# Kernel optimization log

Measured on AMD Instinct MI355X. Metric: run time of the kernel, lower is better.

## Reference

```python
import jax, jax.numpy as jnp
import numpy as np

NUM_GRAPHS = 256
LAMBDA = 0.01


def setup_inputs() -> dict:
    key = jax.random.key(0)
    k1, k2, k3, k4, k5 = jax.random.split(key, 5)
    N, D, E = 100000, 64, 1200000
    logits = jax.random.normal(k1, (NUM_GRAPHS, 10), dtype=jnp.float32)
    labels = jax.random.randint(k2, (NUM_GRAPHS,), 0, 10, dtype=jnp.int64)
    x = jax.random.normal(k3, (N, D), dtype=jnp.float32)
    edge_index = jax.random.randint(k4, (2, E), 0, N, dtype=jnp.int64)
    batch = jnp.sort(jax.random.randint(k5, (N,), 0, NUM_GRAPHS, dtype=jnp.int64))
    return {"logits": logits, "labels": labels, "x": x,
            "edge_index": edge_index, "batch": batch}


def reference(logits, labels, x, edge_index, batch):
    # cross-entropy (mean over graphs)
    logp = jax.nn.log_softmax(logits, axis=-1)
    ce_loss = -jnp.mean(jnp.take_along_axis(logp, labels[:, None], axis=1))

    # Dirichlet energy
    row, col = edge_index[0], edge_index[1]
    N = x.shape[0]
    ones_e = jnp.ones(row.shape, dtype=x.dtype)
    deg = jax.ops.segment_sum(ones_e, row, num_segments=N)          # [N]
    deg_inv_sqrt = jnp.where(deg > 0, jax.lax.rsqrt(jnp.where(deg > 0, deg, 1.0)), 0.0)
    norm = deg_inv_sqrt[row] * deg_inv_sqrt[col]                    # [E]
    diff = x[row] - x[col]                                          # [E, D]
    sq = jnp.sum(diff * diff, axis=1)                               # [E]
    energy_e = norm * sq

    seg = batch[row]                                                # graph id per edge
    energy_sum = jax.ops.segment_sum(energy_e, seg, num_segments=NUM_GRAPHS)
    edge_counts = jax.ops.segment_sum(ones_e, seg, num_segments=NUM_GRAPHS)
    edge_counts = jnp.clip(edge_counts, 1.0, None)
    smoothness_loss = jnp.mean(energy_sum / edge_counts)

    return ce_loss + LAMBDA * smoothness_loss
```

## Files before the change

kernel.cpp:

```cpp
#include <hip/hip_runtime.h>
#include <math.h>

#define NUM_GRAPHS 256
#define LAMBDA 0.01f

typedef int            v4i __attribute__((ext_vector_type(4)));
typedef float          v4f __attribute__((ext_vector_type(4)));
typedef unsigned int   v4u __attribute__((ext_vector_type(4)));
typedef unsigned short v8h __attribute__((ext_vector_type(8)));

__device__ __forceinline__ unsigned short f2bf_rne(float f) {
    unsigned int u = __float_as_uint(f);
    u = u + 0x7fffu + ((u >> 16) & 1u);
    return (unsigned short)(u >> 16);
}

__device__ __forceinline__ float bfdiff_sq(v4u a, v4u b) {
    float s = 0.0f;
    #pragma unroll
    for (int k = 0; k < 4; ++k) {
        float alo = __uint_as_float(a[k] << 16);
        float ahi = __uint_as_float(a[k] & 0xffff0000u);
        float blo = __uint_as_float(b[k] << 16);
        float bhi = __uint_as_float(b[k] & 0xffff0000u);
        float d1 = alo - blo;
        float d2 = ahi - bhi;
        s += d1 * d1;
        s += d2 * d2;
    }
    return s;
}

__global__ void k_cvt(const float* __restrict__ x, v8h* __restrict__ xh,
                      float* __restrict__ zr, int zcount8, long total8) {
    long j = (long)blockIdx.x * blockDim.x + threadIdx.x;
    if (j < total8) {
        const v4f* xp = (const v4f*)(x + j * 8);
        v4f a = xp[0], b = xp[1];
        v8h o;
        o[0] = f2bf_rne(a[0]); o[1] = f2bf_rne(a[1]);
        o[2] = f2bf_rne(a[2]); o[3] = f2bf_rne(a[3]);
        o[4] = f2bf_rne(b[0]); o[5] = f2bf_rne(b[1]);
        o[6] = f2bf_rne(b[2]); o[7] = f2bf_rne(b[3]);
        __builtin_nontemporal_store(o, xh + j);
    }
    if (j < zcount8) {
        v4f z = {0.0f, 0.0f, 0.0f, 0.0f};
        v4f* zp = (v4f*)(zr + j * 8);
        zp[0] = z; zp[1] = z;
    }
}

__global__ void k_deg_v(const int* __restrict__ row, float* __restrict__ deg, int E) {
    const int i = blockIdx.x * blockDim.x + threadIdx.x;
    const int stride = gridDim.x * blockDim.x;
    const int E4 = E >> 2;
    const v4i* r4 = (const v4i*)row;
    for (int k = i; k < E4; k += stride) {
        v4i v = __builtin_nontemporal_load(&r4[k]);
        atomicAdd(&deg[v[0]], 1.0f);
        atomicAdd(&deg[v[1]], 1.0f);
        atomicAdd(&deg[v[2]], 1.0f);
        atomicAdd(&deg[v[3]], 1.0f);
    }
    for (int e = (E4 << 2) + i; e < E; e += stride) {
        atomicAdd(&deg[row[e]], 1.0f);
    }
}

template <bool PACK>
__global__ void k_dis(float* __restrict__ deg_dis, const int* __restrict__ batch,
                      float* __restrict__ cnt, float2* __restrict__ pk, int N) {
    int i = blockIdx.x * blockDim.x + threadIdx.x;
    bool valid = (i < N);
    float d = valid ? deg_dis[i] : 0.0f;
    int g = valid ? batch[i] : -1;
    float dis = (d > 0.0f) ? rsqrtf(d) : 0.0f;
    if (valid) {
        deg_dis[i] = dis;
        if (PACK) pk[i] = make_float2(dis, __int_as_float(g));
    }

    int gmin = g, gmax = g;
    #pragma unroll
    for (int m = 1; m < 64; m <<= 1) {
        gmin = min(gmin, __shfl_xor(gmin, m));
        gmax = max(gmax, __shfl_xor(gmax, m));
    }
    if (gmin == gmax && gmin >= 0) {
        float s = d;
        #pragma unroll
        for (int m = 1; m < 64; m <<= 1) s += __shfl_xor(s, m);
        if ((threadIdx.x & 63) == 0) atomicAdd(&cnt[g], s);
    } else if (valid) {
        atomicAdd(&cnt[g], d);
    }
}

__global__ void k_fused(const int* __restrict__ row, const int* __restrict__ col,
                        const v4u* __restrict__ xh4, const float2* __restrict__ pk,
                        float* __restrict__ g_energy, int E) {
    __shared__ float lbin[NUM_GRAPHS];
    lbin[threadIdx.x] = 0.0f;
    __syncthreads();

    const int lane   = threadIdx.x & 63;
    const int lane8  = lane & 7;
    const int gi     = lane >> 3;
    const int wave   = (blockIdx.x * blockDim.x + threadIdx.x) >> 6;
    const int nwaves = (gridDim.x * blockDim.x) >> 6;
    const int E32    = E >> 5;

    for (int t = wave; t < E32; t += nwaves) {
        const int ebase = t * 32 + gi * 4;

        v4i rv = __builtin_nontemporal_load((const v4i*)(row + ebase));
        v4i cv = __builtin_nontemporal_load((const v4i*)(col + ebase));

        v4u a0 = xh4[(long)rv[0] * 8 + lane8];
        v4u b0 = xh4[(long)cv[0] * 8 + lane8];
        v4u a1 = xh4[(long)rv[1] * 8 + lane8];
        v4u b1 = xh4[(long)cv[1] * 8 + lane8];
        v4u a2 = xh4[(long)rv[2] * 8 + lane8];
        v4u b2 = xh4[(long)cv[2] * 8 + lane8];
        v4u a3 = xh4[(long)rv[3] * 8 + lane8];
        v4u b3 = xh4[(long)cv[3] * 8 + lane8];

        float s0 = bfdiff_sq(a0, b0);
        float s1 = bfdiff_sq(a1, b1);
        float s2 = bfdiff_sq(a2, b2);
        float s3 = bfdiff_sq(a3, b3);

        s0 += __shfl_xor(s0, 1); s1 += __shfl_xor(s1, 1);
        s2 += __shfl_xor(s2, 1); s3 += __shfl_xor(s3, 1);
        s0 += __shfl_xor(s0, 2); s1 += __shfl_xor(s1, 2);
        s2 += __shfl_xor(s2, 2); s3 += __shfl_xor(s3, 2);
        s0 += __shfl_xor(s0, 4); s1 += __shfl_xor(s1, 4);
        s2 += __shfl_xor(s2, 4); s3 += __shfl_xor(s3, 4);

        if (lane8 < 4) {
            int r = rv[lane8];
            int c = cv[lane8];
            float s = (lane8 == 0) ? s0 : (lane8 == 1) ? s1 : (lane8 == 2) ? s2 : s3;
            float2 pr = pk[r];
            float2 pc = pk[c];
            atomicAdd(&lbin[__float_as_int(pr.y)], pr.x * pc.x * s);
        }
    }

    for (int e = (E32 << 5) + wave; e < E; e += nwaves) {
        int r = row[e], c = col[e];
        v4u a = xh4[(long)r * 8 + lane8];
        v4u b = xh4[(long)c * 8 + lane8];
        float s = bfdiff_sq(a, b);
        s += __shfl_xor(s, 1);
        s += __shfl_xor(s, 2);
        s += __shfl_xor(s, 4);
        if (lane == 0) {
            float2 pr = pk[r];
            float2 pc = pk[c];
            atomicAdd(&lbin[__float_as_int(pr.y)], pr.x * pc.x * s);
        }
    }

    __syncthreads();
    float v = lbin[threadIdx.x];
    if (v != 0.0f) atomicAdd(&g_energy[threadIdx.x], v);
}

__global__ void k_deg_sq(const int* __restrict__ row, const int* __restrict__ col,
                         const float4* __restrict__ x4, float* __restrict__ deg,
                         float* __restrict__ sq, int E) {
    const int lane   = threadIdx.x & 63;
    const int lane16 = lane & 15;
    const int wave   = (blockIdx.x * blockDim.x + threadIdx.x) >> 6;
    const int nwaves = (gridDim.x * blockDim.x) >> 6;
    const int gi     = (lane >> 4);
    const int E16    = E >> 4;

    for (int t = wave; t < E16; t += nwaves) {
        const int ebase = t * 16 + gi * 4;

        v4i rv = __builtin_nontemporal_load((const v4i*)(row + ebase));
        v4i cv = __builtin_nontemporal_load((const v4i*)(col + ebase));

        float4 a0 = x4[(long)rv[0] * 16 + lane16];
        float4 b0 = x4[(long)cv[0] * 16 + lane16];
        float4 a1 = x4[(long)rv[1] * 16 + lane16];
        float4 b1 = x4[(long)cv[1] * 16 + lane16];
        float4 a2 = x4[(long)rv[2] * 16 + lane16];
        float4 b2 = x4[(long)cv[2] * 16 + lane16];
        float4 a3 = x4[(long)rv[3] * 16 + lane16];
        float4 b3 = x4[(long)cv[3] * 16 + lane16];

        float dx, dy, dz, dw;
        dx = a0.x - b0.x; dy = a0.y - b0.y; dz = a0.z - b0.z; dw = a0.w - b0.w;
        float s0 = dx * dx + dy * dy + dz * dz + dw * dw;
        dx = a1.x - b1.x; dy = a1.y - b1.y; dz = a1.z - b1.z; dw = a1.w - b1.w;
        float s1 = dx * dx + dy * dy + dz * dz + dw * dw;
        dx = a2.x - b2.x; dy = a2.y - b2.y; dz = a2.z - b2.z; dw = a2.w - b2.w;
        float s2 = dx * dx + dy * dy + dz * dz + dw * dw;
        dx = a3.x - b3.x; dy = a3.y - b3.y; dz = a3.z - b3.z; dw = a3.w - b3.w;
        float s3 = dx * dx + dy * dy + dz * dz + dw * dw;

        s0 += __shfl_xor(s0, 1); s1 += __shfl_xor(s1, 1);
        s2 += __shfl_xor(s2, 1); s3 += __shfl_xor(s3, 1);
        s0 += __shfl_xor(s0, 2); s1 += __shfl_xor(s1, 2);
        s2 += __shfl_xor(s2, 2); s3 += __shfl_xor(s3, 2);
        s0 += __shfl_xor(s0, 4); s1 += __shfl_xor(s1, 4);
        s2 += __shfl_xor(s2, 4); s3 += __shfl_xor(s3, 4);
        s0 += __shfl_xor(s0, 8); s1 += __shfl_xor(s1, 8);
        s2 += __shfl_xor(s2, 8); s3 += __shfl_xor(s3, 8);

        if (lane16 == 0) {
            v4f sv;
            sv[0] = s0; sv[1] = s1; sv[2] = s2; sv[3] = s3;
            __builtin_nontemporal_store(sv, (v4f*)(sq + ebase));
        } else if (lane16 == 1) {
            atomicAdd(&deg[rv[0]], 1.0f);
        } else if (lane16 == 2) {
            atomicAdd(&deg[rv[1]], 1.0f);
        } else if (lane16 == 3) {
            atomicAdd(&deg[rv[2]], 1.0f);
        } else if (lane16 == 4) {
            atomicAdd(&deg[rv[3]], 1.0f);
        }
    }

    for (int e = (E16 << 4) + wave; e < E; e += nwaves) {
        int r = row[e], c = col[e];
        float4 a = x4[(long)r * 16 + lane16];
        float4 b = x4[(long)c * 16 + lane16];
        float dx = a.x - b.x, dy = a.y - b.y, dz = a.z - b.z, dw = a.w - b.w;
        float s = dx * dx + dy * dy + dz * dz + dw * dw;
        s += __shfl_xor(s, 1);
        s += __shfl_xor(s, 2);
        s += __shfl_xor(s, 4);
        s += __shfl_xor(s, 8);
        if (lane == 0) sq[e] = s;
        if (lane == 1) atomicAdd(&deg[r], 1.0f);
    }
}

__global__ void k_bin(const int* __restrict__ row, const int* __restrict__ col,
                      const float* __restrict__ sq, const float2* __restrict__ pk,
                      float* __restrict__ g_energy, int E) {
    __shared__ float lbin[NUM_GRAPHS];
    lbin[threadIdx.x] = 0.0f;
    __syncthreads();

    const int i = blockIdx.x * blockDim.x + threadIdx.x;
    const int stride = gridDim.x * blockDim.x;
    const int E4 = E >> 2;
    const v4i* r4 = (const v4i*)row;
    const v4i* c4 = (const v4i*)col;
    const v4f* s4 = (const v4f*)sq;

    for (int k = i; k < E4; k += stride) {
        v4i r = __builtin_nontemporal_load(&r4[k]);
        v4i c = __builtin_nontemporal_load(&c4[k]);
        v4f s = __builtin_nontemporal_load(&s4[k]);
        float2 pr0 = pk[r[0]], pr1 = pk[r[1]], pr2 = pk[r[2]], pr3 = pk[r[3]];
        float2 pc0 = pk[c[0]], pc1 = pk[c[1]], pc2 = pk[c[2]], pc3 = pk[c[3]];
        atomicAdd(&lbin[__float_as_int(pr0.y)], pr0.x * pc0.x * s[0]);
        atomicAdd(&lbin[__float_as_int(pr1.y)], pr1.x * pc1.x * s[1]);
        atomicAdd(&lbin[__float_as_int(pr2.y)], pr2.x * pc2.x * s[2]);
        atomicAdd(&lbin[__float_as_int(pr3.y)], pr3.x * pc3.x * s[3]);
    }
    for (int e = (E4 << 2) + i; e < E; e += stride) {
        float2 pr = pk[row[e]], pc = pk[col[e]];
        atomicAdd(&lbin[__float_as_int(pr.y)], pr.x * pc.x * sq[e]);
    }

    __syncthreads();
    float v = lbin[threadIdx.x];
    if (v != 0.0f) atomicAdd(&g_energy[threadIdx.x], v);
}

__global__ void k_final(const float* __restrict__ logits, const int* __restrict__ labels,
                        const float* __restrict__ g_energy, const float* __restrict__ cnt,
                        float* __restrict__ out) {
    const int t = threadIdx.x;
    const float* lg = logits + t * 10;

    float m = -INFINITY;
    #pragma unroll
    for (int j = 0; j < 10; ++j) m = fmaxf(m, lg[j]);
    float sum = 0.0f;
    #pragma unroll
    for (int j = 0; j < 10; ++j) sum += expf(lg[j] - m);
    float lse = m + logf(sum);
    float ce = lse - lg[labels[t]];

    float sm = g_energy[t] / fmaxf(cnt[t], 1.0f);

    float v = ce + LAMBDA * sm;
    #pragma unroll
    for (int mk = 1; mk < 64; mk <<= 1) v += __shfl_xor(v, mk);

    __shared__ float wsum[4];
    if ((t & 63) == 0) wsum[t >> 6] = v;
    __syncthreads();
    if (t == 0) out[0] = (wsum[0] + wsum[1] + wsum[2] + wsum[3]) * (1.0f / 256.0f);
}

extern "C" void kernel_launch(void* const* d_in, const int* in_sizes, int n_in,
                              void* d_out, int out_size, void* d_ws, size_t ws_size,
                              hipStream_t stream) {
    const float* logits = (const float*)d_in[0];
    const int* labels   = (const int*)d_in[1];
    const float* x      = (const float*)d_in[2];
    const int* edge_idx = (const int*)d_in[3];
    const int* batch    = (const int*)d_in[4];

    const int N = in_sizes[2] / 64;
    const int E = in_sizes[3] / 2;

    const int* row = edge_idx;
    const int* col = edge_idx + E;

    float*  deg_dis  = (float*)d_ws;
    float*  g_energy = deg_dis + N;
    float*  cnt      = g_energy + NUM_GRAPHS;
    float2* pk_fast  = (float2*)(cnt + NUM_GRAPHS);
    unsigned short* xh = (unsigned short*)(pk_fast + N);

    const size_t base_floats = (size_t)N + 2 * NUM_GRAPHS;
    const size_t need_fast = (base_floats + (size_t)2 * N + (size_t)32 * N) * sizeof(float);

    float*  sq      = (float*)(cnt + NUM_GRAPHS);
    float2* pk_slow = (float2*)(sq + E);
    const size_t need_sq = (base_floats + (size_t)E) * sizeof(float);
    const size_t need_pk = need_sq + (size_t)2 * N * sizeof(float);

    if (ws_size >= need_fast) {
        const long total8 = (long)N * 8;
        const int zcount8 = (int)((N + 2 * NUM_GRAPHS + 7) / 8);
        const int cvt_blocks = (int)((total8 + 255) / 256);
        k_cvt<<<cvt_blocks, 256, 0, stream>>>(x, (v8h*)xh, deg_dis, zcount8, total8);
        k_deg_v<<<1024, 256, 0, stream>>>(row, deg_dis, E);
        k_dis<true><<<(N + 255) / 256, 256, 0, stream>>>(deg_dis, batch, cnt, pk_fast, N);
        k_fused<<<2048, 256, 0, stream>>>(row, col, (const v4u*)xh, pk_fast,
                                          g_energy, E);
    } else if (ws_size >= need_pk) {
        (void)hipMemsetAsync(d_ws, 0, base_floats * sizeof(float), stream);
        k_deg_sq<<<2048, 256, 0, stream>>>(row, col, (const float4*)x, deg_dis, sq, E);
        k_dis<true><<<(N + 255) / 256, 256, 0, stream>>>(deg_dis, batch, cnt, pk_slow, N);
        k_bin<<<512, 256, 0, stream>>>(row, col, sq, pk_slow, g_energy, E);
    } else {
        (void)hipMemsetAsync(d_ws, 0, base_floats * sizeof(float), stream);
        k_deg_v<<<1024, 256, 0, stream>>>(row, deg_dis, E);
        k_dis<false><<<(N + 255) / 256, 256, 0, stream>>>(deg_dis, batch, cnt, pk_slow, N);
        k_bin<<<512, 256, 0, stream>>>(row, col, sq, pk_slow, g_energy, E);
    }
    k_final<<<1, 256, 0, stream>>>(logits, labels, g_energy, cnt, (float*)d_out);
}
```

Before: 247.1 us.

## Fuse degree counting into bf16 gather pass, bin energy in separate pass

The fast path used to run a row-only degree atomic pass and then a fused gather+energy kernel. It now computes squared differences from the bf16 copy of x together with the degree atomics in one k_gather kernel, processing 8 edges per lane group. The per-edge sums go to a workspace array that k_bin later scales and bins. This drops the separate degree pass but adds a write and re-read of an E-sized float array plus a second read of row/col. It also needs more workspace, so the fast path is only taken if ws_size covers sq as well.

```diff
diff --git a/kernel.cpp b/kernel.cpp
--- a/kernel.cpp
+++ b/kernel.cpp
@@ -51,20 +51,85 @@
     }
 }
 
-__global__ void k_deg_v(const int* __restrict__ row, float* __restrict__ deg, int E) {
-    const int i = blockIdx.x * blockDim.x + threadIdx.x;
-    const int stride = gridDim.x * blockDim.x;
-    const int E4 = E >> 2;
-    const v4i* r4 = (const v4i*)row;
-    for (int k = i; k < E4; k += stride) {
-        v4i v = __builtin_nontemporal_load(&r4[k]);
-        atomicAdd(&deg[v[0]], 1.0f);
-        atomicAdd(&deg[v[1]], 1.0f);
-        atomicAdd(&deg[v[2]], 1.0f);
-        atomicAdd(&deg[v[3]], 1.0f);
-    }
-    for (int e = (E4 << 2) + i; e < E; e += stride) {
-        atomicAdd(&deg[row[e]], 1.0f);
+__global__ void __launch_bounds__(256, 4)
+k_gather(const int* __restrict__ row, const int* __restrict__ col,
+         const v4u* __restrict__ xh4, float* __restrict__ deg,
+         float* __restrict__ sq, int E) {
+    const int lane   = threadIdx.x & 63;
+    const int lane8  = lane & 7;
+    const int gi     = lane >> 3;
+    const int wave   = (blockIdx.x * blockDim.x + threadIdx.x) >> 6;
+    const int nwaves = (gridDim.x * blockDim.x) >> 6;
+    const int E64    = E >> 6;
+
+    for (int t = wave; t < E64; t += nwaves) {
+        const int ebase = t * 64 + gi * 8;
+
+        v4i rv0 = __builtin_nontemporal_load((const v4i*)(row + ebase));
+        v4i rv1 = __builtin_nontemporal_load((const v4i*)(row + ebase + 4));
+        v4i cv0 = __builtin_nontemporal_load((const v4i*)(col + ebase));
+        v4i cv1 = __builtin_nontemporal_load((const v4i*)(col + ebase + 4));
+
+        v4u a0 = xh4[(long)rv0[0] * 8 + lane8];
+        v4u b0 = xh4[(long)cv0[0] * 8 + lane8];
+        v4u a1 = xh4[(long)rv0[1] * 8 + lane8];
+        v4u b1 = xh4[(long)cv0[1] * 8 + lane8];
+        v4u a2 = xh4[(long)rv0[2] * 8 + lane8];
+        v4u b2 = xh4[(long)cv0[2] * 8 + lane8];
+        v4u a3 = xh4[(long)rv0[3] * 8 + lane8];
+        v4u b3 = xh4[(long)cv0[3] * 8 + lane8];
+        v4u a4 = xh4[(long)rv1[0] * 8 + lane8];
+        v4u b4 = xh4[(long)cv1[0] * 8 + lane8];
+        v4u a5 = xh4[(long)rv1[1] * 8 + lane8];
+        v4u b5 = xh4[(long)cv1[1] * 8 + lane8];
+        v4u a6 = xh4[(long)rv1[2] * 8 + lane8];
+        v4u b6 = xh4[(long)cv1[2] * 8 + lane8];
+        v4u a7 = xh4[(long)rv1[3] * 8 + lane8];
+        v4u b7 = xh4[(long)cv1[3] * 8 + lane8];
+
+        float s0 = bfdiff_sq(a0, b0);
+        float s1 = bfdiff_sq(a1, b1);
+        float s2 = bfdiff_sq(a2, b2);
+        float s3 = bfdiff_sq(a3, b3);
+        float s4 = bfdiff_sq(a4, b4);
+        float s5 = bfdiff_sq(a5, b5);
+        float s6 = bfdiff_sq(a6, b6);
+        float s7 = bfdiff_sq(a7, b7);
+
+        s0 += __shfl_xor(s0, 1); s1 += __shfl_xor(s1, 1);
+        s2 += __shfl_xor(s2, 1); s3 += __shfl_xor(s3, 1);
+        s4 += __shfl_xor(s4, 1); s5 += __shfl_xor(s5, 1);
+        s6 += __shfl_xor(s6, 1); s7 += __shfl_xor(s7, 1);
+        s0 += __shfl_xor(s0, 2); s1 += __shfl_xor(s1, 2);
+        s2 += __shfl_xor(s2, 2); s3 += __shfl_xor(s3, 2);
+        s4 += __shfl_xor(s4, 2); s5 += __shfl_xor(s5, 2);
+        s6 += __shfl_xor(s6, 2); s7 += __shfl_xor(s7, 2);
+        s0 += __shfl_xor(s0, 4); s1 += __shfl_xor(s1, 4);
+        s2 += __shfl_xor(s2, 4); s3 += __shfl_xor(s3, 4);
+        s4 += __shfl_xor(s4, 4); s5 += __shfl_xor(s5, 4);
+        s6 += __shfl_xor(s6, 4); s7 += __shfl_xor(s7, 4);
+
+        if (lane8 == 0) {
+            v4f sv; sv[0] = s0; sv[1] = s1; sv[2] = s2; sv[3] = s3;
+            __builtin_nontemporal_store(sv, (v4f*)(sq + ebase));
+        } else if (lane8 == 1) {
+            v4f sv; sv[0] = s4; sv[1] = s5; sv[2] = s6; sv[3] = s7;
+            __builtin_nontemporal_store(sv, (v4f*)(sq + ebase + 4));
+        }
+        int rr = (lane8 < 4) ? rv0[lane8] : rv1[lane8 - 4];
+        atomicAdd(&deg[rr], 1.0f);
+    }
+
+    for (int e = (E64 << 6) + wave; e < E; e += nwaves) {
+        int r = row[e], c = col[e];
+        v4u a = xh4[(long)r * 8 + lane8];
+        v4u b = xh4[(long)c * 8 + lane8];
+        float s = bfdiff_sq(a, b);
+        s += __shfl_xor(s, 1);
+        s += __shfl_xor(s, 2);
+        s += __shfl_xor(s, 4);
+        if (lane == 0) sq[e] = s;
+        if (lane == 8) atomicAdd(&deg[r], 1.0f);
     }
 }
 
@@ -97,151 +162,6 @@
     }
 }
 
-__global__ void k_fused(const int* __restrict__ row, const int* __restrict__ col,
-                        const v4u* __restrict__ xh4, const float2* __restrict__ pk,
-                        float* __restrict__ g_energy, int E) {
-    __shared__ float lbin[NUM_GRAPHS];
-    lbin[threadIdx.x] = 0.0f;
-    __syncthreads();
-
-    const int lane   = threadIdx.x & 63;
-    const int lane8  = lane & 7;
-    const int gi     = lane >> 3;
-    const int wave   = (blockIdx.x * blockDim.x + threadIdx.x) >> 6;
-    const int nwaves = (gridDim.x * blockDim.x) >> 6;
-    const int E32    = E >> 5;
-
-    for (int t = wave; t < E32; t += nwaves) {
-        const int ebase = t * 32 + gi * 4;
-
-        v4i rv = __builtin_nontemporal_load((const v4i*)(row + ebase));
-        v4i cv = __builtin_nontemporal_load((const v4i*)(col + ebase));
-
-        v4u a0 = xh4[(long)rv[0] * 8 + lane8];
-        v4u b0 = xh4[(long)cv[0] * 8 + lane8];
-        v4u a1 = xh4[(long)rv[1] * 8 + lane8];
-        v4u b1 = xh4[(long)cv[1] * 8 + lane8];
-        v4u a2 = xh4[(long)rv[2] * 8 + lane8];
-        v4u b2 = xh4[(long)cv[2] * 8 + lane8];
-        v4u a3 = xh4[(long)rv[3] * 8 + lane8];
-        v4u b3 = xh4[(long)cv[3] * 8 + lane8];
-
-        float s0 = bfdiff_sq(a0, b0);
-        float s1 = bfdiff_sq(a1, b1);
-        float s2 = bfdiff_sq(a2, b2);
-        float s3 = bfdiff_sq(a3, b3);
-
-        s0 += __shfl_xor(s0, 1); s1 += __shfl_xor(s1, 1);
-        s2 += __shfl_xor(s2, 1); s3 += __shfl_xor(s3, 1);
-        s0 += __shfl_xor(s0, 2); s1 += __shfl_xor(s1, 2);
-        s2 += __shfl_xor(s2, 2); s3 += __shfl_xor(s3, 2);
-        s0 += __shfl_xor(s0, 4); s1 += __shfl_xor(s1, 4);
-        s2 += __shfl_xor(s2, 4); s3 += __shfl_xor(s3, 4);
-
-        if (lane8 < 4) {
-            int r = rv[lane8];
-            int c = cv[lane8];
-            float s = (lane8 == 0) ? s0 : (lane8 == 1) ? s1 : (lane8 == 2) ? s2 : s3;
-            float2 pr = pk[r];
-            float2 pc = pk[c];
-            atomicAdd(&lbin[__float_as_int(pr.y)], pr.x * pc.x * s);
-        }
-    }
-
-    for (int e = (E32 << 5) + wave; e < E; e += nwaves) {
-        int r = row[e], c = col[e];
-        v4u a = xh4[(long)r * 8 + lane8];
-        v4u b = xh4[(long)c * 8 + lane8];
-        float s = bfdiff_sq(a, b);
-        s += __shfl_xor(s, 1);
-        s += __shfl_xor(s, 2);
-        s += __shfl_xor(s, 4);
-        if (lane == 0) {
-            float2 pr = pk[r];
-            float2 pc = pk[c];
-            atomicAdd(&lbin[__float_as_int(pr.y)], pr.x * pc.x * s);
-        }
-    }
-
-    __syncthreads();
-    float v = lbin[threadIdx.x];
-    if (v != 0.0f) atomicAdd(&g_energy[threadIdx.x], v);
-}
-
-__global__ void k_deg_sq(const int* __restrict__ row, const int* __restrict__ col,
-                         const float4* __restrict__ x4, float* __restrict__ deg,
-                         float* __restrict__ sq, int E) {
-    const int lane   = threadIdx.x & 63;
-    const int lane16 = lane & 15;
-    const int wave   = (blockIdx.x * blockDim.x + threadIdx.x) >> 6;
-    const int nwaves = (gridDim.x * blockDim.x) >> 6;
-    const int gi     = (lane >> 4);
-    const int E16    = E >> 4;
-
-    for (int t = wave; t < E16; t += nwaves) {
-        const int ebase = t * 16 + gi * 4;
-
-        v4i rv = __builtin_nontemporal_load((const v4i*)(row + ebase));
-        v4i cv = __builtin_nontemporal_load((const v4i*)(col + ebase));
-
-        float4 a0 = x4[(long)rv[0] * 16 + lane16];
-        float4 b0 = x4[(long)cv[0] * 16 + lane16];
-        float4 a1 = x4[(long)rv[1] * 16 + lane16];
-        float4 b1 = x4[(long)cv[1] * 16 + lane16];
-        float4 a2 = x4[(long)rv[2] * 16 + lane16];
-        float4 b2 = x4[(long)cv[2] * 16 + lane16];
-        float4 a3 = x4[(long)rv[3] * 16 + lane16];
-        float4 b3 = x4[(long)cv[3] * 16 + lane16];
-
-        float dx, dy, dz, dw;
-        dx = a0.x - b0.x; dy = a0.y - b0.y; dz = a0.z - b0.z; dw = a0.w - b0.w;
-        float s0 = dx * dx + dy * dy + dz * dz + dw * dw;
-        dx = a1.x - b1.x; dy = a1.y - b1.y; dz = a1.z - b1.z; dw = a1.w - b1.w;
-        float s1 = dx * dx + dy * dy + dz * dz + dw * dw;
-        dx = a2.x - b2.x; dy = a2.y - b2.y; dz = a2.z - b2.z; dw = a2.w - b2.w;
-        float s2 = dx * dx + dy * dy + dz * dz + dw * dw;
-        dx = a3.x - b3.x; dy = a3.y - b3.y; dz = a3.z - b3.z; dw = a3.w - b3.w;
-        float s3 = dx * dx + dy * dy + dz * dz + dw * dw;
-
-        s0 += __shfl_xor(s0, 1); s1 += __shfl_xor(s1, 1);
-        s2 += __shfl_xor(s2, 1); s3 += __shfl_xor(s3, 1);
-        s0 += __shfl_xor(s0, 2); s1 += __shfl_xor(s1, 2);
-        s2 += __shfl_xor(s2, 2); s3 += __shfl_xor(s3, 2);
-        s0 += __shfl_xor(s0, 4); s1 += __shfl_xor(s1, 4);
-        s2 += __shfl_xor(s2, 4); s3 += __shfl_xor(s3, 4);
-        s0 += __shfl_xor(s0, 8); s1 += __shfl_xor(s1, 8);
-        s2 += __shfl_xor(s2, 8); s3 += __shfl_xor(s3, 8);
-
-        if (lane16 == 0) {
-            v4f sv;
-            sv[0] = s0; sv[1] = s1; sv[2] = s2; sv[3] = s3;
-            __builtin_nontemporal_store(sv, (v4f*)(sq + ebase));
-        } else if (lane16 == 1) {
-            atomicAdd(&deg[rv[0]], 1.0f);
-        } else if (lane16 == 2) {
-            atomicAdd(&deg[rv[1]], 1.0f);
-        } else if (lane16 == 3) {
-            atomicAdd(&deg[rv[2]], 1.0f);
-        } else if (lane16 == 4) {
-            atomicAdd(&deg[rv[3]], 1.0f);
-        }
-    }
-
-    for (int e = (E16 << 4) + wave; e < E; e += nwaves) {
-        int r = row[e], c = col[e];
-        float4 a = x4[(long)r * 16 + lane16];
-        float4 b = x4[(long)c * 16 + lane16];
-        float dx = a.x - b.x, dy = a.y - b.y, dz = a.z - b.z, dw = a.w - b.w;
-        float s = dx * dx + dy * dy + dz * dz + dw * dw;
-        s += __shfl_xor(s, 1);
-        s += __shfl_xor(s, 2);
-        s += __shfl_xor(s, 4);
-        s += __shfl_xor(s, 8);
-        if (lane == 0) sq[e] = s;
-        if (lane == 1) atomicAdd(&deg[r], 1.0f);
-    }
-}
-
 __global__ void k_bin(const int* __restrict__ row, const int* __restrict__ col,
                       const float* __restrict__ sq, const float2* __restrict__ pk,
                       float* __restrict__ g_energy, int E) {
@@ -277,6 +197,45 @@
     if (v != 0.0f) atomicAdd(&g_energy[threadIdx.x], v);
 }
 
+__global__ void k_deg_f(const int* __restrict__ row, float* __restrict__ deg, int E) {
+    const int i = blockIdx.x * blockDim.x + threadIdx.x;
+    const int stride = gridDim.x * blockDim.x;
+    for (int e = i; e < E; e += stride) atomicAdd(&deg[row[e]], 1.0f);
+}
+
+__global__ void k_energy(const int* __restrict__ row, const int* __restrict__ col,
+                         const float4* __restrict__ x4, const float* __restrict__ dis,
+                         const int* __restrict__ batch, float* __restrict__ g_energy,
+                         int E) {
+    __shared__ float lbin[NUM_GRAPHS];
+    lbin[threadIdx.x] = 0.0f;
+    __syncthreads();
+
+    const int lane16 = threadIdx.x & 15;
+    const int group = (blockIdx.x * blockDim.x + threadIdx.x) >> 4;
+    const int ngroups = (gridDim.x * blockDim.x) >> 4;
+
+    for (int e = group; e < E; e += ngroups) {
+        int r = row[e];
+        int c = col[e];
+        float4 a = x4[(long)r * 16 + lane16];
+        float4 b = x4[(long)c * 16 + lane16];
+        float nr = dis[r] * dis[c];
+        int g = batch[r];
+        float dx = a.x - b.x, dy = a.y - b.y, dz = a.z - b.z, dw = a.w - b.w;
+        float s = dx * dx + dy * dy + dz * dz + dw * dw;
+        s += __shfl_xor(s, 1);
+        s += __shfl_xor(s, 2);
+        s += __shfl_xor(s, 4);
+        s += __shfl_xor(s, 8);
+        if (lane16 == 0) atomicAdd(&lbin[g], nr * s);
+    }
+
+    __syncthreads();
+    float v = lbin[threadIdx.x];
+    if (v != 0.0f) atomicAdd(&g_energy[threadIdx.x], v);
+}
+
 __global__ void k_final(const float* __restrict__ logits, const int* __restrict__ labels,
                         const float* __restrict__ g_energy, const float* __restrict__ cnt,
                         float* __restrict__ out) {
@@ -322,36 +281,29 @@
     float*  deg_dis  = (float*)d_ws;
     float*  g_energy = deg_dis + N;
     float*  cnt      = g_energy + NUM_GRAPHS;
-    float2* pk_fast  = (float2*)(cnt + NUM_GRAPHS);
-    unsigned short* xh = (unsigned short*)(pk_fast + N);
+    float*  sq       = cnt + NUM_GRAPHS;
+    float2* pk       = (float2*)(sq + E);
+    unsigned short* xh = (unsigned short*)(pk + N);
 
     const size_t base_floats = (size_t)N + 2 * NUM_GRAPHS;
-    const size_t need_fast = (base_floats + (size_t)2 * N + (size_t)32 * N) * sizeof(float);
-
-    float*  sq      = (float*)(cnt + NUM_GRAPHS);
-    float2* pk_slow = (float2*)(sq + E);
-    const size_t need_sq = (base_floats + (size_t)E) * sizeof(float);
-    const size_t need_pk = need_sq + (size_t)2 * N * sizeof(float);
+    const size_t need_sq   = (base_floats + (size_t)E) * sizeof(float);
+    const size_t need_pk   = need_sq + (size_t)2 * N * sizeof(float);
+    const size_t need_fast = need_pk + (size_t)N * 64 * sizeof(unsigned short);
 
     if (ws_size >= need_fast) {
         const long total8 = (long)N * 8;
         const int zcount8 = (int)((N + 2 * NUM_GRAPHS + 7) / 8);
         const int cvt_blocks = (int)((total8 + 255) / 256);
         k_cvt<<<cvt_blocks, 256, 0, stream>>>(x, (v8h*)xh, deg_dis, zcount8, total8);
-        k_deg_v<<<1024, 256, 0, stream>>>(row, deg_dis, E);
-        k_dis<true><<<(N + 255) / 256, 256, 0, stream>>>(deg_dis, batch, cnt, pk_fast, N);
-        k_fused<<<2048, 256, 0, stream>>>(row, col, (const v4u*)xh, pk_fast,
-                                          g_energy, E);
-    } else if (ws_size >= need_pk) {
-        (void)hipMemsetAsync(d_ws, 0, base_floats * sizeof(float), stream);
-        k_deg_sq<<<2048, 256, 0, stream>>>(row, col, (const float4*)x, deg_dis, sq, E);
-        k_dis<true><<<(N + 255) / 256, 256, 0, stream>>>(deg_dis, batch, cnt, pk_slow, N);
-        k_bin<<<512, 256, 0, stream>>>(row, col, sq, pk_slow, g_energy, E);
+        k_gather<<<2048, 256, 0, stream>>>(row, col, (const v4u*)xh, deg_dis, sq, E);
+        k_dis<true><<<(N + 255) / 256, 256, 0, stream>>>(deg_dis, batch, cnt, pk, N);
+        k_bin<<<512, 256, 0, stream>>>(row, col, sq, pk, g_energy, E);
     } else {
         (void)hipMemsetAsync(d_ws, 0, base_floats * sizeof(float), stream);
-        k_deg_v<<<1024, 256, 0, stream>>>(row, deg_dis, E);
-        k_dis<false><<<(N + 255) / 256, 256, 0, stream>>>(deg_dis, batch, cnt, pk_slow, N);
-        k_bin<<<512, 256, 0, stream>>>(row, col, sq, pk_slow, g_energy, E);
+        k_deg_f<<<2048, 256, 0, stream>>>(row, deg_dis, E);
+        k_dis<false><<<(N + 255) / 256, 256, 0, stream>>>(deg_dis, batch, cnt, pk, N);
+        k_energy<<<2048, 256, 0, stream>>>(row, col, (const float4*)x, deg_dis, batch,
+                                           g_energy, E);
     }
     k_final<<<1, 256, 0, stream>>>(logits, labels, g_energy, cnt, (float*)d_out);
 }
```

After: 208.5 us. 1.19x faster.
